# Performance work log

Hardware: AMD Instinct MI355X
Metric: run time of the kernel (lower is better)

## Reference

```python
import jax, jax.numpy as jnp
import numpy as np

# Dimensions (must match init_kwargs)
IC = 8    # independent channels (one Linear each)
RC = 8    # regular channels
PC = 8    # parallel channels
G = 4     # shared-weight groups
IPG = 512 // G   # input length per group = 128
OPG = 512 // G   # output length per group = 128
B = 128


def setup_inputs() -> dict:
    key = jax.random.key(0)
    k1, k2, k3 = jax.random.split(key, 3)
    x = jax.random.normal(k1, (B, IC * RC, PC, IPG * G), dtype=jnp.float32)
    # Per-independent-channel Linear weights/biases (torch Linear: y = x @ W.T + b)
    bound = 1.0 / np.sqrt(IPG)
    W = jax.random.uniform(k2, (IC, OPG, IPG), dtype=jnp.float32, minval=-bound, maxval=bound)
    b = jax.random.uniform(k3, (IC, OPG), dtype=jnp.float32, minval=-bound, maxval=bound)
    return {"x": x, "W": W, "b": b}


def reference(x, W, b):
    Bx = x.shape[0]
    # view -> (B, IC, RC, PC, IPG*G); tensor_split along last + stack(dim=-2)
    # is a contiguous reshape -> (B, IC, RC, PC, G, IPG)
    xi = x.reshape(Bx, IC, RC, PC, G, IPG)
    # block-diagonal grouped GEMM: one Linear per independent channel i
    y = jnp.einsum('bicpgk,iok->bicpgo', xi, W) + b[None, :, None, None, None, :]
    # (B, IC, RC, PC, G, OPG) -> (B, IC*RC, PC, G*OPG)
    return y.reshape(Bx, IC * RC, PC, G * OPG)
```

## Files before the change

kernel.cpp:

```cpp
#include <hip/hip_runtime.h>
#include <hip/hip_bf16.h>

typedef __bf16 bf16x8 __attribute__((ext_vector_type(8)));
typedef __bf16 bf16x4 __attribute__((ext_vector_type(4)));
typedef float floatx4 __attribute__((ext_vector_type(4)));

#define IC 8
#define RC 8
#define PC 8
#define G_ 4
#define IPG 128
#define OPG 128

#define WROW 136

__global__ __launch_bounds__(256, 2)
void mcsl_kernel(const float* __restrict__ x,
                 const float* __restrict__ W,
                 const float* __restrict__ bias,
                 float* __restrict__ y)
{
    __shared__ __align__(16) __bf16 Wlds[128 * WROW];
    __shared__ __align__(16) float blds[128];

    const int tid = threadIdx.x;
    const int i = blockIdx.x & 7;
    const int j = blockIdx.x >> 3;

    const float4* Wsrc = (const float4*)(W + (size_t)i * (OPG * IPG));
    #pragma unroll
    for (int it = 0; it < 16; ++it) {
        int idx = tid + it * 256;
        float4 w4 = Wsrc[idx];
        int o  = idx >> 5;
        int k4 = (idx & 31) << 2;
        bf16x4 wq;
        wq[0] = (__bf16)w4.x; wq[1] = (__bf16)w4.y;
        wq[2] = (__bf16)w4.z; wq[3] = (__bf16)w4.w;
        *(bf16x4*)&Wlds[o * WROW + k4] = wq;
    }
    if (tid < 128) blds[tid] = bias[i * OPG + tid];
    __syncthreads();

    const int lane = tid & 63;
    const int wv   = tid >> 6;
    const int nrow = lane & 15;
    const int quad = lane >> 4;

    bf16x8 wfrag[8][4];
    #pragma unroll
    for (int ct = 0; ct < 8; ++ct)
        #pragma unroll
        for (int ks = 0; ks < 4; ++ks)
            wfrag[ct][ks] = *(const bf16x8*)&Wlds[(ct * 16 + nrow) * WROW + ks * 32 + quad * 8];

    const int b = 2 * j + (wv >> 1);
    const size_t slab = ((size_t)(b * (IC * RC) + i * RC)) * (PC * G_ * IPG);
    const int rhalf = (wv & 1) * 128;

    const float4* xs = (const float4*)(x + slab);
    float*        ys = y + slab;

#define TILE_SRC(T) (xs + (size_t)(rhalf + (T) * 16 + nrow) * 32 + quad * 2)

    float4 pfA[8], pfB[8];
    {
        const float4* s0 = TILE_SRC(0);
        const float4* s1 = TILE_SRC(1);
        #pragma unroll
        for (int ks = 0; ks < 4; ++ks) {
            pfA[2 * ks]     = s0[ks * 8];
            pfA[2 * ks + 1] = s0[ks * 8 + 1];
        }
        #pragma unroll
        for (int ks = 0; ks < 4; ++ks) {
            pfB[2 * ks]     = s1[ks * 8];
            pfB[2 * ks + 1] = s1[ks * 8 + 1];
        }
    }

#define TILE_STEP(T, BUF, PREF) do {                                            \
        floatx4 acc[8];                                                         \
        _Pragma("unroll")                                                       \
        for (int ct = 0; ct < 8; ++ct)                                          \
            acc[ct] = *(const floatx4*)&blds[ct * 16 + quad * 4];               \
        const float4* nsrc = (PREF) ? TILE_SRC((T) + 2) : xs;                   \
        _Pragma("unroll")                                                       \
        for (int ks = 0; ks < 4; ++ks) {                                        \
            float4 a0 = BUF[2 * ks], a1 = BUF[2 * ks + 1];                      \
            if (PREF) {                                                         \
                BUF[2 * ks]     = nsrc[ks * 8];                                 \
                BUF[2 * ks + 1] = nsrc[ks * 8 + 1];                             \
            }                                                                   \
            bf16x8 v;                                                           \
            v[0] = (__bf16)a0.x; v[1] = (__bf16)a0.y;                           \
            v[2] = (__bf16)a0.z; v[3] = (__bf16)a0.w;                           \
            v[4] = (__bf16)a1.x; v[5] = (__bf16)a1.y;                           \
            v[6] = (__bf16)a1.z; v[7] = (__bf16)a1.w;                           \
            _Pragma("unroll")                                                   \
            for (int ct = 0; ct < 8; ++ct)                                      \
                acc[ct] = __builtin_amdgcn_mfma_f32_16x16x32_bf16(              \
                              wfrag[ct][ks], v, acc[ct], 0, 0, 0);              \
        }                                                                       \
        float* yrow = ys + (size_t)(rhalf + (T) * 16 + nrow) * OPG + quad * 4;  \
        _Pragma("unroll")                                                       \
        for (int ct = 0; ct < 8; ++ct)                                          \
            __builtin_nontemporal_store(acc[ct], (floatx4*)(yrow + ct * 16));   \
    } while (0)

    TILE_STEP(0, pfA, 1);
    TILE_STEP(1, pfB, 1);
    TILE_STEP(2, pfA, 1);
    TILE_STEP(3, pfB, 1);
    TILE_STEP(4, pfA, 1);
    TILE_STEP(5, pfB, 1);
    TILE_STEP(6, pfA, 0);
    TILE_STEP(7, pfB, 0);

#undef TILE_STEP
#undef TILE_SRC
}

extern "C" void kernel_launch(void* const* d_in, const int* in_sizes, int n_in,
                              void* d_out, int out_size, void* d_ws, size_t ws_size,
                              hipStream_t stream) {
    const float* x = (const float*)d_in[0];
    const float* W = (const float*)d_in[1];
    const float* b = (const float*)d_in[2];
    float* y = (float*)d_out;
    dim3 grid(512), block(256);
    hipLaunchKernelGGL(mcsl_kernel, grid, block, 0, stream, x, W, b, y);
}
```

Baseline: 249.2 us.

## Stream x through double-buffered LDS via direct global-to-LDS loads

Input tiles are now fetched with global_load_lds straight into a two-chunk LDS ring, with explicit vmcnt waits and barriers so chunk c+2 loads while chunk c is computed. Weights are stored in LDS with an XOR swizzle and read per MFMA instead of held as 32 register fragments. Each wave now handles four output column tiles instead of eight. The aim is deeper memory pipelining and lower register pressure, at the cost of extra LDS traffic, block-wide barriers every chunk, and hand-counted wait values that must match the store and load ordering.

```diff
diff --git a/kernel.cpp b/kernel.cpp
--- a/kernel.cpp
+++ b/kernel.cpp
@@ -5,14 +5,10 @@
 typedef __bf16 bf16x4 __attribute__((ext_vector_type(4)));
 typedef float floatx4 __attribute__((ext_vector_type(4)));
 
-#define IC 8
-#define RC 8
-#define PC 8
-#define G_ 4
-#define IPG 128
-#define OPG 128
+#define AS1 __attribute__((address_space(1)))
+#define AS3 __attribute__((address_space(3)))
 
-#define WROW 136
+#define CHUNK_B 16384
 
 __global__ __launch_bounds__(256, 2)
 void mcsl_kernel(const float* __restrict__ x,
@@ -20,105 +16,123 @@
                  const float* __restrict__ bias,
                  float* __restrict__ y)
 {
-    __shared__ __align__(16) __bf16 Wlds[128 * WROW];
+    __shared__ __align__(16) unsigned char Wl[32768];
+    __shared__ __align__(16) unsigned char Xl[2 * CHUNK_B];
     __shared__ __align__(16) float blds[128];
 
-    const int tid = threadIdx.x;
-    const int i = blockIdx.x & 7;
-    const int j = blockIdx.x >> 3;
-
-    const float4* Wsrc = (const float4*)(W + (size_t)i * (OPG * IPG));
-    #pragma unroll
-    for (int it = 0; it < 16; ++it) {
-        int idx = tid + it * 256;
-        float4 w4 = Wsrc[idx];
-        int o  = idx >> 5;
-        int k4 = (idx & 31) << 2;
-        bf16x4 wq;
-        wq[0] = (__bf16)w4.x; wq[1] = (__bf16)w4.y;
-        wq[2] = (__bf16)w4.z; wq[3] = (__bf16)w4.w;
-        *(bf16x4*)&Wlds[o * WROW + k4] = wq;
-    }
-    if (tid < 128) blds[tid] = bias[i * OPG + tid];
-    __syncthreads();
-
+    const int tid  = threadIdx.x;
+    const int i    = blockIdx.x & 7;
+    const int j    = blockIdx.x >> 3;
     const int lane = tid & 63;
     const int wv   = tid >> 6;
     const int nrow = lane & 15;
     const int quad = lane >> 4;
 
-    bf16x8 wfrag[8][4];
-    #pragma unroll
-    for (int ct = 0; ct < 8; ++ct)
+    {
+        const float4* Wsrc = (const float4*)(W + (size_t)i * (128 * 128));
         #pragma unroll
-        for (int ks = 0; ks < 4; ++ks)
-            wfrag[ct][ks] = *(const bf16x8*)&Wlds[(ct * 16 + nrow) * WROW + ks * 32 + quad * 8];
-
-    const int b = 2 * j + (wv >> 1);
-    const size_t slab = ((size_t)(b * (IC * RC) + i * RC)) * (PC * G_ * IPG);
-    const int rhalf = (wv & 1) * 128;
-
-    const float4* xs = (const float4*)(x + slab);
-    float*        ys = y + slab;
-
-#define TILE_SRC(T) (xs + (size_t)(rhalf + (T) * 16 + nrow) * 32 + quad * 2)
-
-    float4 pfA[8], pfB[8];
-    {
-        const float4* s0 = TILE_SRC(0);
-        const float4* s1 = TILE_SRC(1);
-        #pragma unroll
-        for (int ks = 0; ks < 4; ++ks) {
-            pfA[2 * ks]     = s0[ks * 8];
-            pfA[2 * ks + 1] = s0[ks * 8 + 1];
+        for (int it = 0; it < 16; ++it) {
+            int idx = tid + it * 256;
+            float4 w4 = Wsrc[idx];
+            int o  = idx >> 5;
+            int b8 = (idx & 31) << 3;
+            int sw = b8 ^ ((o & 7) << 4);
+            bf16x4 wq;
+            wq[0] = (__bf16)w4.x; wq[1] = (__bf16)w4.y;
+            wq[2] = (__bf16)w4.z; wq[3] = (__bf16)w4.w;
+            *(bf16x4*)&Wl[o * 256 + sw] = wq;
         }
-        #pragma unroll
-        for (int ks = 0; ks < 4; ++ks) {
-            pfB[2 * ks]     = s1[ks * 8];
-            pfB[2 * ks + 1] = s1[ks * 8 + 1];
-        }
+        if (tid < 128) blds[tid] = bias[i * 128 + tid];
     }
 
-#define TILE_STEP(T, BUF, PREF) do {                                            \
-        floatx4 acc[8];                                                         \
+    const size_t xoff0 = ((size_t)(2 * j)     * 64 + i * 8) * 4096;
+    const size_t xoff1 = ((size_t)(2 * j + 1) * 64 + i * 8) * 4096;
+
+#define STAGE(c) do {                                                            \
+        const unsigned char* gb =                                               \
+            (const unsigned char*)(x + (((c) & 8) ? xoff1 : xoff0))             \
+            + (size_t)((c) & 7) * CHUNK_B;                                      \
+        unsigned char* db = Xl + ((c) & 1) * CHUNK_B;                           \
         _Pragma("unroll")                                                       \
-        for (int ct = 0; ct < 8; ++ct)                                          \
-            acc[ct] = *(const floatx4*)&blds[ct * 16 + quad * 4];               \
-        const float4* nsrc = (PREF) ? TILE_SRC((T) + 2) : xs;                   \
+        for (int jj = 0; jj < 4; ++jj) {                                        \
+            const int Lu = (jj * 256 + wv * 64) * 16;    \
+            const int L  = Lu + lane * 16;                                      \
+            const int rr = L >> 9;                                              \
+            const int sb = (L & 511) ^ ((rr & 7) << 4);                         \
+            __builtin_amdgcn_global_load_lds(                                   \
+                (AS1 void*)(gb + (size_t)rr * 512 + sb),                        \
+                (AS3 void*)(db + Lu), 16, 0, 0);                                \
+        }                                                                       \
+    } while (0)
+
+    const int rloc = (wv >> 1) * 16 + nrow;
+    const int ctb  = (wv & 1) * 4;
+    const int xrow = rloc * 512;
+    const int rsw  = (rloc & 7) << 4;
+    const unsigned char* wrow = Wl + nrow * 256 + ctb * 4096;
+    const int wsw = (nrow & 7) << 4;
+
+#define COMPUTE(c) do {                                                          \
+        const unsigned char* bb = Xl + ((c) & 1) * CHUNK_B;                     \
+        floatx4 acc0 = *(const floatx4*)&blds[(ctb + 0) * 16 + quad * 4];       \
+        floatx4 acc1 = *(const floatx4*)&blds[(ctb + 1) * 16 + quad * 4];       \
+        floatx4 acc2 = *(const floatx4*)&blds[(ctb + 2) * 16 + quad * 4];       \
+        floatx4 acc3 = *(const floatx4*)&blds[(ctb + 3) * 16 + quad * 4];       \
         _Pragma("unroll")                                                       \
         for (int ks = 0; ks < 4; ++ks) {                                        \
-            float4 a0 = BUF[2 * ks], a1 = BUF[2 * ks + 1];                      \
-            if (PREF) {                                                         \
-                BUF[2 * ks]     = nsrc[ks * 8];                                 \
-                BUF[2 * ks + 1] = nsrc[ks * 8 + 1];                             \
-            }                                                                   \
-            bf16x8 v;                                                           \
-            v[0] = (__bf16)a0.x; v[1] = (__bf16)a0.y;                           \
-            v[2] = (__bf16)a0.z; v[3] = (__bf16)a0.w;                           \
-            v[4] = (__bf16)a1.x; v[5] = (__bf16)a1.y;                           \
-            v[6] = (__bf16)a1.z; v[7] = (__bf16)a1.w;                           \
-            _Pragma("unroll")                                                   \
-            for (int ct = 0; ct < 8; ++ct)                                      \
-                acc[ct] = __builtin_amdgcn_mfma_f32_16x16x32_bf16(              \
-                              wfrag[ct][ks], v, acc[ct], 0, 0, 0);              \
+            const int kb = ks * 128 + quad * 32;                                \
+            floatx4 xa = *(const floatx4*)(bb + xrow + ((kb)      ^ rsw));      \
+            floatx4 xb = *(const floatx4*)(bb + xrow + ((kb + 16) ^ rsw));      \
+            bf16x8 xf;                                                          \
+            xf[0] = (__bf16)xa.x; xf[1] = (__bf16)xa.y;                         \
+            xf[2] = (__bf16)xa.z; xf[3] = (__bf16)xa.w;                         \
+            xf[4] = (__bf16)xb.x; xf[5] = (__bf16)xb.y;                         \
+            xf[6] = (__bf16)xb.z; xf[7] = (__bf16)xb.w;                         \
+            const unsigned char* wp = wrow + ((ks * 64 + quad * 16) ^ wsw);     \
+            acc0 = __builtin_amdgcn_mfma_f32_16x16x32_bf16(                     \
+                       *(const bf16x8*)(wp),         xf, acc0, 0, 0, 0);        \
+            acc1 = __builtin_amdgcn_mfma_f32_16x16x32_bf16(                     \
+                       *(const bf16x8*)(wp + 4096),  xf, acc1, 0, 0, 0);        \
+            acc2 = __builtin_amdgcn_mfma_f32_16x16x32_bf16(                     \
+                       *(const bf16x8*)(wp + 8192),  xf, acc2, 0, 0, 0);        \
+            acc3 = __builtin_amdgcn_mfma_f32_16x16x32_bf16(                     \
+                       *(const bf16x8*)(wp + 12288), xf, acc3, 0, 0, 0);        \
         }                                                                       \
-        float* yrow = ys + (size_t)(rhalf + (T) * 16 + nrow) * OPG + quad * 4;  \
-        _Pragma("unroll")                                                       \
-        for (int ct = 0; ct < 8; ++ct)                                          \
-            __builtin_nontemporal_store(acc[ct], (floatx4*)(yrow + ct * 16));   \
+        float* yr = y + (((c) & 8) ? xoff1 : xoff0)                             \
+                  + (size_t)(((c) & 7) * 32 + rloc) * 128 + ctb * 16 + quad * 4;\
+        __builtin_nontemporal_store(acc0, (floatx4*)(yr));                      \
+        __builtin_nontemporal_store(acc1, (floatx4*)(yr + 16));                 \
+        __builtin_nontemporal_store(acc2, (floatx4*)(yr + 32));                 \
+        __builtin_nontemporal_store(acc3, (floatx4*)(yr + 48));                 \
     } while (0)
 
-    TILE_STEP(0, pfA, 1);
-    TILE_STEP(1, pfB, 1);
-    TILE_STEP(2, pfA, 1);
-    TILE_STEP(3, pfB, 1);
-    TILE_STEP(4, pfA, 1);
-    TILE_STEP(5, pfB, 1);
-    TILE_STEP(6, pfA, 0);
-    TILE_STEP(7, pfB, 0);
+#define TAIL(WNLIT, DOSTAGE, c) do {                                            \
+        __builtin_amdgcn_sched_barrier(0);                                      \
+        __builtin_amdgcn_s_barrier();                                           \
+        if (DOSTAGE) STAGE((c) + 2);                                            \
+        asm volatile("s_waitcnt vmcnt(" WNLIT ")" ::: "memory");                \
+        __builtin_amdgcn_sched_barrier(0);                                      \
+        __builtin_amdgcn_s_barrier();                                           \
+    } while (0)
 
-#undef TILE_STEP
-#undef TILE_SRC
+    STAGE(0);
+    STAGE(1);
+    asm volatile("s_waitcnt vmcnt(4) lgkmcnt(0)" ::: "memory");
+    __builtin_amdgcn_sched_barrier(0);
+    __builtin_amdgcn_s_barrier();
+
+    #pragma unroll 2
+    for (int c = 0; c < 14; ++c) {
+        COMPUTE(c);
+        TAIL("8", 1, c);
+    }
+    COMPUTE(14);
+    TAIL("4", 0, 14);
+    COMPUTE(15);
+
+#undef STAGE
+#undef COMPUTE
+#undef TAIL
 }
 
 extern "C" void kernel_launch(void* const* d_in, const int* in_sizes, int n_in,
```

Measured after the change: 250.2 us. No clear change (+0.4%).
